# Kernel tuning notes

Measured on AMD Instinct MI355X. Metric: run time of the kernel, lower is better.

Reference implementation:

```python
import jax, jax.numpy as jnp
import numpy as np

H_SIZE = 2048
N_HEADS = 16
N_KV = 8
HEAD_DIM = 128
INTER = 8192
WINDOW = 1024
ROPE_BASE = 10000.0
EPS = 1e-6
import math
LAYER_SCALAR_INIT = math.sqrt(1.0 / 8)


def rms_norm(x, w, eps=EPS):
    var = jnp.mean(x * x, axis=-1, keepdims=True)
    return x * jax.lax.rsqrt(var + eps) * w


def rope(x, pos):
    # x: [B,S,H,D], pos: [S]
    half = HEAD_DIM // 2
    inv_freq = 1.0 / (ROPE_BASE ** (jnp.arange(0, HEAD_DIM, 2, dtype=jnp.float32) / HEAD_DIM))
    freqs = pos[:, None].astype(jnp.float32) * inv_freq[None, :]  # [S, D/2]
    cos = jnp.concatenate([jnp.cos(freqs), jnp.cos(freqs)], axis=-1)[None, :, None, :]
    sin = jnp.concatenate([jnp.sin(freqs), jnp.sin(freqs)], axis=-1)[None, :, None, :]
    x1, x2 = x[..., :half], x[..., half:]
    rot = jnp.concatenate([-x2, x1], axis=-1)
    return x * cos + rot * sin


def setup_inputs() -> dict:
    key = jax.random.key(0)
    ks = jax.random.split(key, 12)
    B, S = 2, 2048
    std = 0.02
    return {
        "x": jax.random.normal(ks[0], (B, S, H_SIZE), dtype=jnp.float32),
        "wq": jax.random.normal(ks[1], (N_HEADS * HEAD_DIM, H_SIZE), dtype=jnp.float32) * std,
        "wk": jax.random.normal(ks[2], (N_KV * HEAD_DIM, H_SIZE), dtype=jnp.float32) * std,
        "wv": jax.random.normal(ks[3], (N_KV * HEAD_DIM, H_SIZE), dtype=jnp.float32) * std,
        "wo": jax.random.normal(ks[4], (H_SIZE, N_HEADS * HEAD_DIM), dtype=jnp.float32) * std,
        "w_in_norm": jnp.ones((H_SIZE,), jnp.float32),
        "w_post_attn_norm": jnp.ones((H_SIZE,), jnp.float32),
        "w_pre_ffn_norm": jnp.ones((H_SIZE,), jnp.float32),
        "w_post_ffn_norm": jnp.ones((H_SIZE,), jnp.float32),
        "w_gate": jax.random.normal(ks[5], (INTER, H_SIZE), dtype=jnp.float32) * std,
        "w_up": jax.random.normal(ks[6], (INTER, H_SIZE), dtype=jnp.float32) * std,
        "w_down": jax.random.normal(ks[7], (H_SIZE, INTER), dtype=jnp.float32) * std,
        "layer_scalar": jnp.full((1,), LAYER_SCALAR_INIT, dtype=jnp.float32),
    }


def _block(x, wq, wk, wv, wo, w_in_norm, w_post_attn_norm, w_pre_ffn_norm,
           w_post_ffn_norm, w_gate, w_up, w_down, layer_scalar):
    B, S, _ = x.shape
    h = rms_norm(x, w_in_norm)

    # --- sliding-window GQA attention with RoPE ---
    q = (h @ wq.T).reshape(B, S, N_HEADS, HEAD_DIM)
    k = (h @ wk.T).reshape(B, S, N_KV, HEAD_DIM)
    v = (h @ wv.T).reshape(B, S, N_KV, HEAD_DIM)
    pos = jnp.arange(S)
    q = rope(q, pos)
    k = rope(k, pos)
    group = N_HEADS // N_KV
    k = jnp.repeat(k, group, axis=2)  # [B,S,H,D]
    v = jnp.repeat(v, group, axis=2)
    scale = 1.0 / jnp.sqrt(jnp.float32(HEAD_DIM))
    scores = jnp.einsum('bihd,bjhd->bhij', q, k) * scale  # [B,H,S,S]
    i = pos[:, None]
    j = pos[None, :]
    mask = (j <= i) & (i - j < WINDOW)  # causal sliding window
    scores = jnp.where(mask[None, None], scores, jnp.finfo(scores.dtype).min)
    probs = jax.nn.softmax(scores, axis=-1)
    attn = jnp.einsum('bhij,bjhd->bihd', probs, v).reshape(B, S, N_HEADS * HEAD_DIM)
    attn_out = attn @ wo.T

    h = x + rms_norm(attn_out, w_post_attn_norm)

    # --- GeGLU FFN (exact gelu, matching F.gelu default) ---
    ffn_in = rms_norm(h, w_pre_ffn_norm)
    gate = jax.nn.gelu(ffn_in @ w_gate.T, approximate=False)
    up = ffn_in @ w_up.T
    ffn_out = (gate * up) @ w_down.T
    h = h + rms_norm(ffn_out, w_post_ffn_norm)

    return h * layer_scalar


def reference(x, wq, wk, wv, wo, w_in_norm, w_post_attn_norm, w_pre_ffn_norm,
              w_post_ffn_norm, w_gate, w_up, w_down, layer_scalar):
    return _block(x, wq, wk, wv, wo, w_in_norm, w_post_attn_norm, w_pre_ffn_norm,
                  w_post_ffn_norm, w_gate, w_up, w_down, layer_scalar)
```

## Files before the change

kernel.cpp:

```cpp
#include <hip/hip_runtime.h>


typedef unsigned short u16;
typedef __attribute__((ext_vector_type(4))) float f32x4;
typedef __attribute__((ext_vector_type(8))) short bf16x8;

#define HSZ   2048
#define NH    16
#define NKV   8
#define HD    128
#define INTER 8192
#define SEQ   2048
#define BATCH 2
#define MTOK  (BATCH*SEQ)
#define WIN   1024

__device__ __forceinline__ u16 f2bf(float f) {
    union { float f; unsigned int u; } c; c.f = f;
    unsigned int u = c.u;
    u += 0x7fffu + ((u >> 16) & 1u);
    return (u16)(u >> 16);
}
__device__ __forceinline__ float bf2f(u16 v) {
    union { unsigned int u; float f; } c; c.u = ((unsigned int)v) << 16;
    return c.f;
}
__device__ __forceinline__ float sq4(float4 v) {
    return v.x*v.x + v.y*v.y + v.z*v.z + v.w*v.w;
}
__device__ __forceinline__ void async_ld16(const void* g, void* l) {
    __builtin_amdgcn_global_load_lds(
        (const __attribute__((address_space(1))) void*)g,
        (__attribute__((address_space(3))) void*)l, 16, 0, 0);
}
__device__ __forceinline__ float fast_erf(float x) {
    float ax = fabsf(x);
    float t = 1.0f / (1.0f + 0.3275911f * ax);
    float y = t * (0.254829592f + t * (-0.284496736f + t * (1.421413741f +
              t * (-1.453152027f + t * 1.061405429f))));
    float e = 1.0f - y * __expf(-x * x);
    return copysignf(e, x);
}

__global__ __launch_bounds__(256) void cvt_f32_bf16_k(const float* __restrict__ src,
                                                      u16* __restrict__ dst, int n4) {
    int i = blockIdx.x * 256 + threadIdx.x;
    if (i >= n4) return;
    float4 v = ((const float4*)src)[i];
    ushort4 o;
    o.x = f2bf(v.x); o.y = f2bf(v.y); o.z = f2bf(v.z); o.w = f2bf(v.w);
    ((ushort4*)dst)[i] = o;
}

__global__ __launch_bounds__(256) void cvt_gu_k(const float* __restrict__ wg,
                                                const float* __restrict__ wu,
                                                u16* __restrict__ dst) {
    long i4 = ((long)blockIdx.x * 256 + threadIdx.x) * 4;
    int r = (int)(i4 >> 11);
    int c = (int)(i4 & 2047);
    const float* srow = ((r & 1) ? wu : wg) + (long)(r >> 1) * HSZ + c;
    float4 v = *(const float4*)srow;
    ushort4 o;
    o.x = f2bf(v.x); o.y = f2bf(v.y); o.z = f2bf(v.z); o.w = f2bf(v.w);
    *(ushort4*)(dst + i4) = o;
}

__global__ __launch_bounds__(256) void rmsnorm_bf16_k(const float* __restrict__ x,
                                                      const float* __restrict__ w,
                                                      u16* __restrict__ out) {
    const int row = blockIdx.x, t = threadIdx.x;
    __shared__ float sb[4];
    const float4* xr = (const float4*)(x + (long)row * HSZ);
    float4 v0 = xr[t], v1 = xr[t + 256];
    float ss = sq4(v0) + sq4(v1);
#pragma unroll
    for (int o = 32; o; o >>= 1) ss += __shfl_xor(ss, o);
    if ((t & 63) == 0) sb[t >> 6] = ss;
    __syncthreads();
    ss = sb[0] + sb[1] + sb[2] + sb[3];
    const float rs = rsqrtf(ss * (1.f / HSZ) + 1e-6f);
    const float4* wr = (const float4*)w;
    float4 w0 = wr[t], w1 = wr[t + 256];
    ushort4 o0, o1;
    o0.x = f2bf(v0.x * rs * w0.x); o0.y = f2bf(v0.y * rs * w0.y);
    o0.z = f2bf(v0.z * rs * w0.z); o0.w = f2bf(v0.w * rs * w0.w);
    o1.x = f2bf(v1.x * rs * w1.x); o1.y = f2bf(v1.y * rs * w1.y);
    o1.z = f2bf(v1.z * rs * w1.z); o1.w = f2bf(v1.w * rs * w1.w);
    ushort4* orow = (ushort4*)(out + (long)row * HSZ);
    orow[t] = o0; orow[t + 256] = o1;
}

template <int EPI>
__global__ __launch_bounds__(256) void gemm_bt(const u16* __restrict__ A,
                                               const u16* __restrict__ Bw,
                                               u16* __restrict__ outp,
                                               int N, int K) {
    __shared__ alignas(16) u16 As[128 * 32];
    __shared__ alignas(16) u16 Bs[128 * 32];
    const int tid  = threadIdx.x;
    const int wave = tid >> 6;
    const int lane = tid & 63;
    const int m0 = blockIdx.x << 7;
    const int n0 = blockIdx.y << 7;
    const int wm = (wave & 1) << 6;
    const int wn = (wave >> 1) << 6;
    const int lrow = lane & 15;
    const int px = ((lane >> 4) ^ ((lrow >> 1) & 3)) << 3;

    f32x4 acc[4][4] = {};

    const int c0 = tid, c1 = tid + 256;
    const int sc0 = (((c0 & 3) ^ ((c0 >> 3) & 3)) << 3);
    const int sc1 = (((c1 & 3) ^ ((c1 >> 3) & 3)) << 3);
    const u16* a0p = A  + (long)(m0 + (c0 >> 2)) * K + sc0;
    const u16* a1p = A  + (long)(m0 + (c1 >> 2)) * K + sc1;
    const u16* b0p = Bw + (long)(n0 + (c0 >> 2)) * K + sc0;
    const u16* b1p = Bw + (long)(n0 + (c1 >> 2)) * K + sc1;
    u16* as0 = As + (wave << 9);
    u16* as1 = As + 2048 + (wave << 9);
    u16* bs0 = Bs + (wave << 9);
    u16* bs1 = Bs + 2048 + (wave << 9);

    for (int k0 = 0; k0 < K; k0 += 32) {
        __syncthreads();
        async_ld16(a0p + k0, as0);
        async_ld16(a1p + k0, as1);
        async_ld16(b0p + k0, bs0);
        async_ld16(b1p + k0, bs1);
        __syncthreads();
        bf16x8 af[4], bfr[4];
#pragma unroll
        for (int mi = 0; mi < 4; ++mi)
            af[mi] = *(const bf16x8*)(As + ((wm + mi * 16 + lrow) << 5) + px);
#pragma unroll
        for (int ni = 0; ni < 4; ++ni)
            bfr[ni] = *(const bf16x8*)(Bs + ((wn + ni * 16 + lrow) << 5) + px);
#pragma unroll
        for (int mi = 0; mi < 4; ++mi)
#pragma unroll
            for (int ni = 0; ni < 4; ++ni)
                acc[mi][ni] = __builtin_amdgcn_mfma_f32_16x16x32_bf16(
                    af[mi], bfr[ni], acc[mi][ni], 0, 0, 0);
    }

    const int drow = (lane >> 4) << 2;
    if constexpr (EPI == 1) {
#pragma unroll
        for (int mi = 0; mi < 4; ++mi) {
            const int rb = m0 + wm + mi * 16 + drow;
#pragma unroll
            for (int ni = 0; ni < 4; ++ni) {
                const int col = n0 + wn + ni * 16 + lrow;
#pragma unroll
                for (int r = 0; r < 4; ++r)
                    outp[(long)(rb + r) * N + col] = f2bf(acc[mi][ni][r]);
            }
        }
    } else {
        const int No = N >> 1;
#pragma unroll
        for (int mi = 0; mi < 4; ++mi) {
            const int rb = m0 + wm + mi * 16 + drow;
#pragma unroll
            for (int ni = 0; ni < 4; ni += 2) {
                const int colown = n0 + wn + (ni + (lane & 1)) * 16 + lrow;
#pragma unroll
                for (int r = 0; r < 4; ++r) {
                    float a = acc[mi][ni][r];
                    float b = acc[mi][ni + 1][r];
                    float a1 = __shfl_xor(a, 1);
                    float b1 = __shfl_xor(b, 1);
                    float g = (lane & 1) ? b1 : a;
                    float u = (lane & 1) ? b  : a1;
                    float act = 0.5f * g * (1.f + fast_erf(g * 0.70710678f)) * u;
                    outp[(long)(rb + r) * No + (colown >> 1)] = f2bf(act);
                }
            }
        }
    }
}

__global__ __launch_bounds__(128) void rope_repack_k(const u16* __restrict__ qkv,
                                                     u16* __restrict__ Qh,
                                                     u16* __restrict__ Kh) {
    const int m = blockIdx.x;
    const int slot = blockIdx.y;
    const int d = threadIdx.x;
    const int b = m >> 11, s = m & 2047;
    const int colbase = (slot < 16) ? (slot << 7) : (2048 + ((slot - 16) << 7));
    const float xv = bf2f(qkv[(long)m * 4096 + colbase + d]);
    const float xp = bf2f(qkv[(long)m * 4096 + colbase + (d ^ 64)]);
    const int i = d & 63;
    const float inv = exp2f(-(float)i * 0.20762050593045864f);
    const float fr = (float)s * inv;
    const float cs = cosf(fr), sn = sinf(fr);
    const float ov = (d < 64) ? (xv * cs - xp * sn) : (xv * cs + xp * sn);
    if (slot < 16) {
        Qh[(((long)(b * NH + slot)) * SEQ + s) * HD + d] = f2bf(ov);
    } else {
        Kh[(((long)(b * NKV + (slot - 16))) * SEQ + s) * HD + d] = f2bf(ov);
    }
}

__global__ __launch_bounds__(256) void v_transpose_k(const u16* __restrict__ qkv,
                                                     u16* __restrict__ Vt) {
    __shared__ alignas(16) u16 tile[64][130];
    const int st = blockIdx.x, g = blockIdx.y, b = blockIdx.z;
    const int s0 = st * 64;
    const int tid = threadIdx.x;
#pragma unroll
    for (int i = 0; i < 32; ++i) {
        int idx = i * 256 + tid;
        int sl = idx >> 7, d = idx & 127;
        tile[sl][d] = qkv[(long)(b * SEQ + s0 + sl) * 4096 + 3072 + g * 128 + d];
    }
    __syncthreads();
#pragma unroll
    for (int i = 0; i < 32; ++i) {
        int idx = i * 256 + tid;
        int d = idx >> 6, sl = idx & 63;
        Vt[((long)(b * NKV + g) * HD + d) * SEQ + s0 + sl] = tile[sl][d];
    }
}

__global__ __launch_bounds__(256) void flash_attn_k(const u16* __restrict__ Qh,
                                                    const u16* __restrict__ Kh,
                                                    const u16* __restrict__ Vt,
                                                    u16* __restrict__ attn) {
    __shared__ alignas(16) u16 Qs[64 * 128];
    __shared__ alignas(16) u16 Ks[64 * 128];
    __shared__ alignas(16) u16 Vts[128 * 64];
    __shared__ alignas(16) u16 Ps[4][16 * 64];
    const int tid = threadIdx.x;
    const int wave = tid >> 6, lane = tid & 63;
    const int qt = blockIdx.x, h = blockIdx.y, b = blockIdx.z;
    const int g = h >> 1;
    const int q0 = qt * 64;
    const u16* Qg = Qh + (((long)(b * NH + h) * SEQ) + q0) * HD;
    const u16* Kg = Kh + ((long)(b * NKV + g) * SEQ) * HD;
    const u16* Vg = Vt + ((long)(b * NKV + g) * HD) * SEQ;

    {
        const int4* src = (const int4*)Qg;
        int4* dst = (int4*)Qs;
#pragma unroll
        for (int i = 0; i < 4; ++i) dst[tid + i * 256] = src[tid + i * 256];
    }
    __syncthreads();
    const int lrow = lane & 15;
    const int kq = (lane >> 4) << 3;
    bf16x8 aq[4];
#pragma unroll
    for (int ks = 0; ks < 4; ++ks)
        aq[ks] = *(const bf16x8*)(Qs + (wave * 16 + lrow) * 128 + ks * 32 + kq);

    f32x4 o[8] = {};
    float mrow[4], lsum[4];
#pragma unroll
    for (int r = 0; r < 4; ++r) { mrow[r] = -1e30f; lsum[r] = 0.f; }

    const int jlo = (q0 - (WIN - 1)) > 0 ? (q0 - (WIN - 1)) : 0;
    const int t0 = jlo >> 6, t1 = q0 >> 6;
    for (int jt = t0; jt <= t1; ++jt) {
        const int j0 = jt * 64;
        __syncthreads();
        {
            const int4* src = (const int4*)(Kg + (long)j0 * HD);
            int4* dst = (int4*)Ks;
#pragma unroll
            for (int i = 0; i < 4; ++i) dst[tid + i * 256] = src[tid + i * 256];
        }
        {
            const int row = tid >> 1, half = tid & 1;
            const int4* src = (const int4*)(Vg + (long)row * SEQ + j0 + half * 32);
            int4* dst = (int4*)(Vts + row * 64 + half * 32);
#pragma unroll
            for (int i = 0; i < 4; ++i) dst[i] = src[i];
        }
        __syncthreads();

        f32x4 sc[4];
#pragma unroll
        for (int nt = 0; nt < 4; ++nt) {
            f32x4 s = {};
#pragma unroll
            for (int ks = 0; ks < 4; ++ks) {
                bf16x8 bk = *(const bf16x8*)(Ks + (nt * 16 + lrow) * 128 + ks * 32 + kq);
                s = __builtin_amdgcn_mfma_f32_16x16x32_bf16(aq[ks], bk, s, 0, 0, 0);
            }
            sc[nt] = s;
        }

        const int qbase = q0 + wave * 16 + ((lane >> 4) << 2);
        float pv[4][4];
#pragma unroll
        for (int r = 0; r < 4; ++r) {
            const int qi = qbase + r;
            float mx = -1e30f;
#pragma unroll
            for (int nt = 0; nt < 4; ++nt) {
                const int ki = j0 + nt * 16 + lrow;
                float s = sc[nt][r] * 0.08838834764831845f;
                bool valid = (ki <= qi) && (qi - ki < WIN);
                s = valid ? s : -1e30f;
                sc[nt][r] = s;
                mx = fmaxf(mx, s);
            }
            mx = fmaxf(mx, __shfl_xor(mx, 1));
            mx = fmaxf(mx, __shfl_xor(mx, 2));
            mx = fmaxf(mx, __shfl_xor(mx, 4));
            mx = fmaxf(mx, __shfl_xor(mx, 8));
            const float mn = fmaxf(mrow[r], mx);
            const float alpha = __expf(mrow[r] - mn);
            float rsum = 0.f;
#pragma unroll
            for (int nt = 0; nt < 4; ++nt) {
                float s = sc[nt][r];
                float p = (s > -1e29f) ? __expf(s - mn) : 0.f;
                pv[nt][r] = p;
                rsum += p;
            }
            rsum += __shfl_xor(rsum, 1);
            rsum += __shfl_xor(rsum, 2);
            rsum += __shfl_xor(rsum, 4);
            rsum += __shfl_xor(rsum, 8);
            lsum[r] = lsum[r] * alpha + rsum;
            mrow[r] = mn;
#pragma unroll
            for (int dt = 0; dt < 8; ++dt) o[dt][r] *= alpha;
        }

        u16* myP = (u16*)Ps[wave];
#pragma unroll
        for (int r = 0; r < 4; ++r) {
            const int prow = ((lane >> 4) << 2) + r;
#pragma unroll
            for (int nt = 0; nt < 4; ++nt)
                myP[prow * 64 + nt * 16 + lrow] = f2bf(pv[nt][r]);
        }
        __syncthreads();

#pragma unroll
        for (int kst = 0; kst < 2; ++kst) {
            bf16x8 ap = *(const bf16x8*)(myP + lrow * 64 + kst * 32 + kq);
#pragma unroll
            for (int dt = 0; dt < 8; ++dt) {
                bf16x8 bv = *(const bf16x8*)(Vts + (dt * 16 + lrow) * 64 + kst * 32 + kq);
                o[dt] = __builtin_amdgcn_mfma_f32_16x16x32_bf16(ap, bv, o[dt], 0, 0, 0);
            }
        }
    }

#pragma unroll
    for (int r = 0; r < 4; ++r) {
        const int qi = q0 + wave * 16 + ((lane >> 4) << 2) + r;
        const float inv = 1.f / lsum[r];
        const long mrowg = (long)b * SEQ + qi;
#pragma unroll
        for (int dt = 0; dt < 8; ++dt)
            attn[mrowg * (NH * HD) + h * 128 + dt * 16 + lrow] = f2bf(o[dt][r] * inv);
    }
}

__global__ __launch_bounds__(256) void addnorm2_k(const float* __restrict__ x,
                                                  const u16* __restrict__ ao,
                                                  const float* __restrict__ wpost,
                                                  const float* __restrict__ wpre,
                                                  u16* __restrict__ h2,
                                                  u16* __restrict__ ffin) {
    const int row = blockIdx.x, t = threadIdx.x;
    __shared__ float sb[4];
    const long base = (long)row * HSZ;
    ushort4 a4_0 = ((const ushort4*)(ao + base))[t];
    ushort4 a4_1 = ((const ushort4*)(ao + base))[t + 256];
    float4 a0, a1;
    a0.x = bf2f(a4_0.x); a0.y = bf2f(a4_0.y); a0.z = bf2f(a4_0.z); a0.w = bf2f(a4_0.w);
    a1.x = bf2f(a4_1.x); a1.y = bf2f(a4_1.y); a1.z = bf2f(a4_1.z); a1.w = bf2f(a4_1.w);
    float ss = sq4(a0) + sq4(a1);
#pragma unroll
    for (int o = 32; o; o >>= 1) ss += __shfl_xor(ss, o);
    if ((t & 63) == 0) sb[t >> 6] = ss;
    __syncthreads();
    ss = sb[0] + sb[1] + sb[2] + sb[3];
    const float rs1 = rsqrtf(ss * (1.f / HSZ) + 1e-6f);

    const float4* xr = (const float4*)(x + base);
    float4 x0 = xr[t], x1 = xr[t + 256];
    float4 wp0 = ((const float4*)wpost)[t], wp1 = ((const float4*)wpost)[t + 256];
    float4 h0, h1;
    h0.x = x0.x + a0.x * rs1 * wp0.x; h0.y = x0.y + a0.y * rs1 * wp0.y;
    h0.z = x0.z + a0.z * rs1 * wp0.z; h0.w = x0.w + a0.w * rs1 * wp0.w;
    h1.x = x1.x + a1.x * rs1 * wp1.x; h1.y = x1.y + a1.y * rs1 * wp1.y;
    h1.z = x1.z + a1.z * rs1 * wp1.z; h1.w = x1.w + a1.w * rs1 * wp1.w;
    ushort4 hb0, hb1;
    hb0.x = f2bf(h0.x); hb0.y = f2bf(h0.y); hb0.z = f2bf(h0.z); hb0.w = f2bf(h0.w);
    hb1.x = f2bf(h1.x); hb1.y = f2bf(h1.y); hb1.z = f2bf(h1.z); hb1.w = f2bf(h1.w);
    ((ushort4*)(h2 + base))[t] = hb0;
    ((ushort4*)(h2 + base))[t + 256] = hb1;

    float ss2 = sq4(h0) + sq4(h1);
#pragma unroll
    for (int o = 32; o; o >>= 1) ss2 += __shfl_xor(ss2, o);
    __syncthreads();
    if ((t & 63) == 0) sb[t >> 6] = ss2;
    __syncthreads();
    ss2 = sb[0] + sb[1] + sb[2] + sb[3];
    const float rs2 = rsqrtf(ss2 * (1.f / HSZ) + 1e-6f);
    float4 wq0 = ((const float4*)wpre)[t], wq1 = ((const float4*)wpre)[t + 256];
    ushort4 o0, o1;
    o0.x = f2bf(h0.x * rs2 * wq0.x); o0.y = f2bf(h0.y * rs2 * wq0.y);
    o0.z = f2bf(h0.z * rs2 * wq0.z); o0.w = f2bf(h0.w * rs2 * wq0.w);
    o1.x = f2bf(h1.x * rs2 * wq1.x); o1.y = f2bf(h1.y * rs2 * wq1.y);
    o1.z = f2bf(h1.z * rs2 * wq1.z); o1.w = f2bf(h1.w * rs2 * wq1.w);
    ushort4* fr = (ushort4*)(ffin + base);
    fr[t] = o0; fr[t + 256] = o1;
}

__global__ __launch_bounds__(256) void final_k(const u16* __restrict__ h2,
                                               const u16* __restrict__ fo,
                                               const float* __restrict__ wpost,
                                               const float* __restrict__ lscal,
                                               float* __restrict__ out) {
    const int row = blockIdx.x, t = threadIdx.x;
    __shared__ float sb[4];
    const long base = (long)row * HSZ;
    ushort4 f4_0 = ((const ushort4*)(fo + base))[t];
    ushort4 f4_1 = ((const ushort4*)(fo + base))[t + 256];
    float4 f0, f1;
    f0.x = bf2f(f4_0.x); f0.y = bf2f(f4_0.y); f0.z = bf2f(f4_0.z); f0.w = bf2f(f4_0.w);
    f1.x = bf2f(f4_1.x); f1.y = bf2f(f4_1.y); f1.z = bf2f(f4_1.z); f1.w = bf2f(f4_1.w);
    float ss = sq4(f0) + sq4(f1);
#pragma unroll
    for (int o = 32; o; o >>= 1) ss += __shfl_xor(ss, o);
    if ((t & 63) == 0) sb[t >> 6] = ss;
    __syncthreads();
    ss = sb[0] + sb[1] + sb[2] + sb[3];
    const float rs = rsqrtf(ss * (1.f / HSZ) + 1e-6f);
    const float sc = lscal[0];
    ushort4 h4_0 = ((const ushort4*)(h2 + base))[t];
    ushort4 h4_1 = ((const ushort4*)(h2 + base))[t + 256];
    float4 wp0 = ((const float4*)wpost)[t], wp1 = ((const float4*)wpost)[t + 256];
    float4 r0, r1;
    r0.x = (bf2f(h4_0.x) + f0.x * rs * wp0.x) * sc;
    r0.y = (bf2f(h4_0.y) + f0.y * rs * wp0.y) * sc;
    r0.z = (bf2f(h4_0.z) + f0.z * rs * wp0.z) * sc;
    r0.w = (bf2f(h4_0.w) + f0.w * rs * wp0.w) * sc;
    r1.x = (bf2f(h4_1.x) + f1.x * rs * wp1.x) * sc;
    r1.y = (bf2f(h4_1.y) + f1.y * rs * wp1.y) * sc;
    r1.z = (bf2f(h4_1.z) + f1.z * rs * wp1.z) * sc;
    r1.w = (bf2f(h4_1.w) + f1.w * rs * wp1.w) * sc;
    ((float4*)(out + base))[t] = r0;
    ((float4*)(out + base))[t + 256] = r1;
}

extern "C" void kernel_launch(void* const* d_in, const int* in_sizes, int n_in,
                              void* d_out, int out_size, void* d_ws, size_t ws_size,
                              hipStream_t stream) {
    (void)in_sizes; (void)n_in; (void)out_size;
    const float* x     = (const float*)d_in[0];
    const float* wq    = (const float*)d_in[1];
    const float* wk    = (const float*)d_in[2];
    const float* wv    = (const float*)d_in[3];
    const float* wo    = (const float*)d_in[4];
    const float* w_in  = (const float*)d_in[5];
    const float* w_pa  = (const float*)d_in[6];
    const float* w_pf  = (const float*)d_in[7];
    const float* w_pff = (const float*)d_in[8];
    const float* wgate = (const float*)d_in[9];
    const float* wup   = (const float*)d_in[10];
    const float* wdown = (const float*)d_in[11];
    const float* lscal = (const float*)d_in[12];
    float* out = (float*)d_out;

    const size_t NEED = 276824064ull;
    if (ws_size < NEED) return;
    char* ws = (char*)d_ws;
    u16* Wqkv  = (u16*)(ws);
    u16* Wo    = (u16*)(ws + 16777216);
    u16* Wgu   = (u16*)(ws + 25165824);
    u16* Wdown = (u16*)(ws + 92274688);
    u16* act   = (u16*)(ws + 125829120);
    u16* R1    = (u16*)(ws + 192937984);
    u16* R2    = (u16*)(ws + 226492416);
    u16* R3    = (u16*)(ws + 260046848);
    u16* qkvb = R1;
    u16* aout = R1;
    u16* ffin = R1 + 8388608;
    u16* fout = R1 + 8388608;
    u16* Qh = R2;
    u16* Kh = R2 + 8388608;
    u16* Vt = R2 + 12582912;
    u16* h2 = R2;
    u16* hnorm = R3;
    u16* attn  = R3;

    cvt_f32_bf16_k<<<4096, 256, 0, stream>>>(wq, Wqkv, 2048 * 2048 / 4);
    cvt_f32_bf16_k<<<2048, 256, 0, stream>>>(wk, Wqkv + 2048 * 2048, 1024 * 2048 / 4);
    cvt_f32_bf16_k<<<2048, 256, 0, stream>>>(wv, Wqkv + 3072 * 2048, 1024 * 2048 / 4);
    cvt_f32_bf16_k<<<4096, 256, 0, stream>>>(wo, Wo, 2048 * 2048 / 4);
    cvt_gu_k<<<32768, 256, 0, stream>>>(wgate, wup, Wgu);
    cvt_f32_bf16_k<<<16384, 256, 0, stream>>>(wdown, Wdown, HSZ * INTER / 4);

    rmsnorm_bf16_k<<<MTOK, 256, 0, stream>>>(x, w_in, hnorm);
    gemm_bt<1><<<dim3(MTOK / 128, 4096 / 128), 256, 0, stream>>>(hnorm, Wqkv, qkvb, 4096, HSZ);
    rope_repack_k<<<dim3(MTOK, 24), 128, 0, stream>>>(qkvb, Qh, Kh);
    v_transpose_k<<<dim3(SEQ / 64, NKV, BATCH), 256, 0, stream>>>(qkvb, Vt);
    flash_attn_k<<<dim3(SEQ / 64, NH, BATCH), 256, 0, stream>>>(Qh, Kh, Vt, attn);
    gemm_bt<1><<<dim3(MTOK / 128, HSZ / 128), 256, 0, stream>>>(attn, Wo, aout, HSZ, HSZ);
    addnorm2_k<<<MTOK, 256, 0, stream>>>(x, aout, w_pa, w_pf, h2, ffin);
    gemm_bt<2><<<dim3(MTOK / 128, 2 * INTER / 128), 256, 0, stream>>>(ffin, Wgu, act, 2 * INTER, HSZ);
    gemm_bt<1><<<dim3(MTOK / 128, HSZ / 128), 256, 0, stream>>>(act, Wdown, fout, HSZ, INTER);
    final_k<<<MTOK, 256, 0, stream>>>(h2, fout, w_pff, lscal, out);
}
```

Before: 1.263 ms.

## Replace GEMM with 4-stage async-pipelined 256-row tile kernel and block swizzle

Replaces the single-buffered 128x128 GEMM with a 512-thread kernel using 256xBN tiles, a 4-deep shared-memory ring of async global-to-LDS loads, and explicit vmcnt waits and barriers. This lets loads overlap MFMA work. It also splits each k-tile into two halves with priority raising around the MFMA bursts, and swizzles block order for L2 locality. The trade is much higher LDS use (up to 128KB per block) and register pressure from 8xNF accumulators, which limits occupancy. The hand-counted wait counts must match the number of loads in flight.

```diff
diff --git a/kernel.cpp b/kernel.cpp
--- a/kernel.cpp
+++ b/kernel.cpp
@@ -90,84 +90,147 @@
     orow[t] = o0; orow[t + 256] = o1;
 }
 
-template <int EPI>
-__global__ __launch_bounds__(256) void gemm_bt(const u16* __restrict__ A,
-                                               const u16* __restrict__ Bw,
-                                               u16* __restrict__ outp,
-                                               int N, int K) {
-    __shared__ alignas(16) u16 As[128 * 32];
-    __shared__ alignas(16) u16 Bs[128 * 32];
+
+#define VM_WAIT(n) asm volatile("s_waitcnt vmcnt(" #n ")" ::: "memory")
+
+#define STAGE_A(pb_, kt_) { \
+    const u16* s_ = Ag + (long)(kt_) * 32; \
+    u16* d_ = (u16*)As + (pb_) * ATILE + (wave << 9); \
+    async_ld16(s_, d_); \
+    async_ld16(s_ + (long)128 * K, d_ + 4096); }
+
+#define STAGE_B(pb_, kt_) { \
+    const u16* s_ = Bg + (long)(kt_) * 32; \
+    u16* d_ = (u16*)Bs + (pb_) * BTILE + (wave << 9); \
+    async_ld16(s_, d_); \
+    if constexpr (NF == 4) { async_ld16(s_ + (long)128 * K, d_ + 4096); } }
+
+#define KTILE(t_, DOSTAGE_, VMW_) { \
+    const int buf_ = (t_) & 3; \
+    const u16* Ab_ = (const u16*)As + buf_ * ATILE; \
+    const u16* Bb_ = (const u16*)Bs + buf_ * BTILE; \
+    const int pf_ = (t_) + 3; \
+    const int pb_ = pf_ & 3; \
+    bf16x8 af[4]; \
+     \
+    _Pragma("unroll") \
+    for (int mi = 0; mi < 4; ++mi) \
+        af[mi] = *(const bf16x8*)(Ab_ + aoff + mi * 512); \
+    _Pragma("unroll") \
+    for (int ni = 0; ni < NF; ++ni) \
+        bfr[ni] = *(const bf16x8*)(Bb_ + boff + ni * 512); \
+    if (DOSTAGE_) { STAGE_A(pb_, pf_); } \
+    __builtin_amdgcn_sched_barrier(0); \
+    __builtin_amdgcn_s_barrier(); \
+    __builtin_amdgcn_s_setprio(1); \
+    _Pragma("unroll") \
+    for (int mi = 0; mi < 4; ++mi) \
+        _Pragma("unroll") \
+        for (int ni = 0; ni < NF; ++ni) \
+            acc[mi][ni] = __builtin_amdgcn_mfma_f32_16x16x32_bf16( \
+                af[mi], bfr[ni], acc[mi][ni], 0, 0, 0); \
+    __builtin_amdgcn_s_setprio(0); \
+    __builtin_amdgcn_sched_barrier(0); \
+    __builtin_amdgcn_s_barrier(); \
+     \
+    _Pragma("unroll") \
+    for (int mi = 0; mi < 4; ++mi) \
+        af[mi] = *(const bf16x8*)(Ab_ + aoff + 2048 + mi * 512); \
+    if (DOSTAGE_) { STAGE_B(pb_, pf_); } \
+    VMW_; \
+    __builtin_amdgcn_sched_barrier(0); \
+    __builtin_amdgcn_s_barrier(); \
+    __builtin_amdgcn_s_setprio(1); \
+    _Pragma("unroll") \
+    for (int mi = 0; mi < 4; ++mi) \
+        _Pragma("unroll") \
+        for (int ni = 0; ni < NF; ++ni) \
+            acc[4 + mi][ni] = __builtin_amdgcn_mfma_f32_16x16x32_bf16( \
+                af[mi], bfr[ni], acc[4 + mi][ni], 0, 0, 0); \
+    __builtin_amdgcn_s_setprio(0); \
+    __builtin_amdgcn_sched_barrier(0); \
+    __builtin_amdgcn_s_barrier(); \
+}
+
+template <int NF, int EPI>
+__global__ __launch_bounds__(512, 2) void gemm_pipe(const u16* __restrict__ A,
+                                                    const u16* __restrict__ Bw,
+                                                    u16* __restrict__ outp,
+                                                    int N, int K) {
+    constexpr int BN    = NF * 64;
+    constexpr int ATILE = 256 * 32;
+    constexpr int BTILE = BN * 32;
+    __shared__ alignas(16) u16 As[4 * ATILE];
+    __shared__ alignas(16) u16 Bs[4 * BTILE];
+
     const int tid  = threadIdx.x;
     const int wave = tid >> 6;
     const int lane = tid & 63;
-    const int m0 = blockIdx.x << 7;
-    const int n0 = blockIdx.y << 7;
-    const int wm = (wave & 1) << 6;
-    const int wn = (wave >> 1) << 6;
+    const int wm   = wave >> 2;
+    const int wn   = wave & 3;
+
+    const int nwg  = gridDim.x * gridDim.y;
+    const int orig = blockIdx.y * gridDim.x + blockIdx.x;
+    const int swz  = (orig & 7) * (nwg >> 3) + (orig >> 3);
+    const int m0   = (swz % gridDim.x) << 8;
+    const int n0   = (swz / gridDim.x) * BN;
+
     const int lrow = lane & 15;
-    const int px = ((lane >> 4) ^ ((lrow >> 1) & 3)) << 3;
-
-    f32x4 acc[4][4] = {};
-
-    const int c0 = tid, c1 = tid + 256;
-    const int sc0 = (((c0 & 3) ^ ((c0 >> 3) & 3)) << 3);
-    const int sc1 = (((c1 & 3) ^ ((c1 >> 3) & 3)) << 3);
-    const u16* a0p = A  + (long)(m0 + (c0 >> 2)) * K + sc0;
-    const u16* a1p = A  + (long)(m0 + (c1 >> 2)) * K + sc1;
-    const u16* b0p = Bw + (long)(n0 + (c0 >> 2)) * K + sc0;
-    const u16* b1p = Bw + (long)(n0 + (c1 >> 2)) * K + sc1;
-    u16* as0 = As + (wave << 9);
-    u16* as1 = As + 2048 + (wave << 9);
-    u16* bs0 = Bs + (wave << 9);
-    u16* bs1 = Bs + 2048 + (wave << 9);
-
-    for (int k0 = 0; k0 < K; k0 += 32) {
-        __syncthreads();
-        async_ld16(a0p + k0, as0);
-        async_ld16(a1p + k0, as1);
-        async_ld16(b0p + k0, bs0);
-        async_ld16(b1p + k0, bs1);
-        __syncthreads();
-        bf16x8 af[4], bfr[4];
-#pragma unroll
-        for (int mi = 0; mi < 4; ++mi)
-            af[mi] = *(const bf16x8*)(As + ((wm + mi * 16 + lrow) << 5) + px);
-#pragma unroll
-        for (int ni = 0; ni < 4; ++ni)
-            bfr[ni] = *(const bf16x8*)(Bs + ((wn + ni * 16 + lrow) << 5) + px);
-#pragma unroll
-        for (int mi = 0; mi < 4; ++mi)
-#pragma unroll
-            for (int ni = 0; ni < 4; ++ni)
-                acc[mi][ni] = __builtin_amdgcn_mfma_f32_16x16x32_bf16(
-                    af[mi], bfr[ni], acc[mi][ni], 0, 0, 0);
-    }
+    const int px   = (((lane >> 4) ^ ((lrow >> 1) & 3)) << 3);
+    const int aoff = ((wm << 7) + lrow) * 32 + px;
+    const int boff = (wn * (NF * 16) + lrow) * 32 + px;
+
+    const int srow = tid >> 2;
+    const int scol = (((tid & 3) ^ ((tid >> 3) & 3)) << 3);
+    const u16* Ag = A  + (long)(m0 + srow) * K + scol;
+    const u16* Bg = Bw + (long)(n0 + srow) * K + scol;
+
+    f32x4 acc[8][NF] = {};
+    bf16x8 bfr[NF];
+
+    const int NT = K >> 5;
+    constexpr int LPT = (NF == 4) ? 4 : 3;
+
+    STAGE_A(0, 0); STAGE_B(0, 0);
+    STAGE_A(1, 1); STAGE_B(1, 1);
+    STAGE_A(2, 2); STAGE_B(2, 2);
+    if constexpr (NF == 4) { VM_WAIT(8); } else { VM_WAIT(6); }
+    __builtin_amdgcn_s_barrier();
+
+    for (int t = 0; t < NT - 3; ++t) {
+        if constexpr (NF == 4) { KTILE(t, 1, VM_WAIT(8)); }
+        else                   { KTILE(t, 1, VM_WAIT(6)); }
+    }
+    if constexpr (NF == 4) { KTILE((NT - 3), 0, VM_WAIT(4)); }
+    else                   { KTILE((NT - 3), 0, VM_WAIT(3)); }
+    KTILE((NT - 2), 0, VM_WAIT(0));
+    KTILE((NT - 1), 0, ((void)0));
 
     const int drow = (lane >> 4) << 2;
     if constexpr (EPI == 1) {
 #pragma unroll
-        for (int mi = 0; mi < 4; ++mi) {
-            const int rb = m0 + wm + mi * 16 + drow;
-#pragma unroll
-            for (int ni = 0; ni < 4; ++ni) {
-                const int col = n0 + wn + ni * 16 + lrow;
+        for (int mi8 = 0; mi8 < 8; ++mi8) {
+            const int rb = m0 + (wm << 7) + ((mi8 >> 2) << 6) + ((mi8 & 3) << 4) + drow;
+#pragma unroll
+            for (int ni = 0; ni < NF; ++ni) {
+                const int col = n0 + wn * (NF * 16) + ni * 16 + lrow;
 #pragma unroll
                 for (int r = 0; r < 4; ++r)
-                    outp[(long)(rb + r) * N + col] = f2bf(acc[mi][ni][r]);
+                    outp[(long)(rb + r) * N + col] = f2bf(acc[mi8][ni][r]);
             }
         }
     } else {
         const int No = N >> 1;
 #pragma unroll
-        for (int mi = 0; mi < 4; ++mi) {
-            const int rb = m0 + wm + mi * 16 + drow;
-#pragma unroll
-            for (int ni = 0; ni < 4; ni += 2) {
-                const int colown = n0 + wn + (ni + (lane & 1)) * 16 + lrow;
+        for (int mi8 = 0; mi8 < 8; ++mi8) {
+            const int rb = m0 + (wm << 7) + ((mi8 >> 2) << 6) + ((mi8 & 3) << 4) + drow;
+#pragma unroll
+            for (int ni = 0; ni < NF; ni += 2) {
+                const int colown = n0 + wn * 64 + (ni + (lane & 1)) * 16 + lrow;
 #pragma unroll
                 for (int r = 0; r < 4; ++r) {
-                    float a = acc[mi][ni][r];
-                    float b = acc[mi][ni + 1][r];
+                    float a = acc[mi8][ni][r];
+                    float b = acc[mi8][ni + 1][r];
                     float a1 = __shfl_xor(a, 1);
                     float b1 = __shfl_xor(b, 1);
                     float g = (lane & 1) ? b1 : a;
@@ -502,13 +565,13 @@
     cvt_f32_bf16_k<<<16384, 256, 0, stream>>>(wdown, Wdown, HSZ * INTER / 4);
 
     rmsnorm_bf16_k<<<MTOK, 256, 0, stream>>>(x, w_in, hnorm);
-    gemm_bt<1><<<dim3(MTOK / 128, 4096 / 128), 256, 0, stream>>>(hnorm, Wqkv, qkvb, 4096, HSZ);
+    gemm_pipe<4, 1><<<dim3(16, 16), 512, 0, stream>>>(hnorm, Wqkv, qkvb, 4096, HSZ);
     rope_repack_k<<<dim3(MTOK, 24), 128, 0, stream>>>(qkvb, Qh, Kh);
     v_transpose_k<<<dim3(SEQ / 64, NKV, BATCH), 256, 0, stream>>>(qkvb, Vt);
     flash_attn_k<<<dim3(SEQ / 64, NH, BATCH), 256, 0, stream>>>(Qh, Kh, Vt, attn);
-    gemm_bt<1><<<dim3(MTOK / 128, HSZ / 128), 256, 0, stream>>>(attn, Wo, aout, HSZ, HSZ);
+    gemm_pipe<2, 1><<<dim3(16, 16), 512, 0, stream>>>(attn, Wo, aout, HSZ, HSZ);
     addnorm2_k<<<MTOK, 256, 0, stream>>>(x, aout, w_pa, w_pf, h2, ffin);
-    gemm_bt<2><<<dim3(MTOK / 128, 2 * INTER / 128), 256, 0, stream>>>(ffin, Wgu, act, 2 * INTER, HSZ);
-    gemm_bt<1><<<dim3(MTOK / 128, HSZ / 128), 256, 0, stream>>>(act, Wdown, fout, HSZ, INTER);
+    gemm_pipe<4, 2><<<dim3(16, 64), 512, 0, stream>>>(ffin, Wgu, act, 2 * INTER, HSZ);
+    gemm_pipe<2, 1><<<dim3(16, 16), 512, 0, stream>>>(act, Wdown, fout, HSZ, INTER);
     final_k<<<MTOK, 256, 0, stream>>>(h2, fout, w_pff, lscal, out);
 }
```

Measured after the change: 1.291 ms. 2.2% more time.
